# Kernel tuning notes

Hardware: AMD Instinct MI355X
Metric: run time of the kernel (lower is better)

Reference implementation:

```python
import jax, jax.numpy as jnp
import numpy as np

MARGIN = 0.8
L_INTRA = 0.1
L_INTER = 0.1
NUM_CLASSES = 64
BIG = 1e30  # finite stand-in for +/-inf so masked reductions stay NaN-free


def _pairwise(x, y):
    xn = jnp.sum(x * x, axis=1, keepdims=True)
    yn = jnp.sum(y * y, axis=1, keepdims=True)
    d2 = xn - 2.0 * (x @ y.T) + yn.T
    return jnp.sqrt(jnp.maximum(d2, 1e-8))


def _loss(anchor, positive, negative, anchor_labels, negative_labels):
    B = anchor.shape[0]
    # plain triplet term on squared distances (as in the original forward)
    pos_d2 = jnp.sum((anchor - positive) ** 2, axis=1)
    neg_d2 = jnp.sum((anchor - negative) ** 2, axis=1)
    triplet = jnp.maximum(pos_d2 - neg_d2 + MARGIN, 0.0)

    emb = jnp.concatenate([anchor, positive, negative], axis=0)                 # [3B, D]
    labels = jnp.concatenate([anchor_labels, anchor_labels, negative_labels])  # [3B]
    N = emb.shape[0]
    dist = _pairwise(emb, emb)                                                  # [3B, 3B]
    dB = dist[:B]                                                               # [B, 3B] rows for the B anchors

    idx = jnp.arange(N)
    pos_mask = (labels[None, :] == anchor_labels[:, None]) & (idx[None, :] != jnp.arange(B)[:, None])
    neg_mask = labels[None, :] != anchor_labels[:, None]
    has_pos = jnp.any(pos_mask, axis=1)
    has_neg = jnp.any(neg_mask, axis=1)

    # batch-hard mining: hardest positive (max) / hardest negative (min) per anchor
    hp = jnp.max(jnp.where(pos_mask, dB, -BIG), axis=1)
    hn = jnp.min(jnp.where(neg_mask, dB, BIG), axis=1)
    hard_valid = has_pos & has_neg
    hard_loss = jnp.where(hard_valid, jnp.maximum(hp - hn + MARGIN, 0.0), 0.0)
    hard_cnt = jnp.sum(hard_valid.astype(jnp.float32))
    hard_mean = jnp.where(hard_cnt > 0, jnp.sum(hard_loss) / jnp.maximum(hard_cnt, 1.0), 0.0)

    # semi-hard mining: for each positive distance p, min negative in (p, p + margin).
    # That min equals the smallest negative strictly greater than p (via searchsorted
    # on the sorted negatives), accepted only if it is also < p + margin.
    neg_sorted = jnp.sort(jnp.where(neg_mask, dB, BIG), axis=1)                 # [B, 3B]
    ins = jax.vmap(lambda s, q: jnp.searchsorted(s, q, side='right'))(neg_sorted, dB)
    cand = jnp.take_along_axis(neg_sorted, jnp.minimum(ins, N - 1), axis=1)
    sh_valid = pos_mask & (ins < N) & (cand < BIG) & (cand < dB + MARGIN)
    sh_loss = jnp.where(sh_valid, jnp.maximum(dB - cand + MARGIN, 0.0), 0.0)
    sh_cnt = jnp.sum(sh_valid.astype(jnp.float32))
    sh_mean = jnp.where(sh_cnt > 0, jnp.sum(sh_loss) / jnp.maximum(sh_cnt, 1.0), 0.0)

    # class-pair distance sums via one-hot projection: T[c1, c2] = sum of dist between
    # members of class c1 and c2 (diagonal = within-class sums, incl. self-pairs, as in torch)
    onehot = (labels[:, None] == jnp.arange(NUM_CLASSES)[None, :]).astype(dist.dtype)  # [3B, C]
    T = onehot.T @ dist @ onehot                                                # [C, C]
    counts = jnp.sum(onehot, axis=0)                                            # [C]
    in_anchor = jnp.zeros(NUM_CLASSES, dtype=bool).at[anchor_labels].set(True)

    intra_valid = in_anchor & (counts > 1)
    intra = jnp.sum(jnp.where(intra_valid, jnp.diag(T) / jnp.maximum(counts * (counts - 1.0), 1.0), 0.0))

    pair_n = counts[:, None] * counts[None, :]
    mean_inter = T / jnp.maximum(pair_n, 1.0)
    c = jnp.arange(NUM_CLASSES)
    pair_mask = in_anchor[:, None] & in_anchor[None, :] & (c[:, None] < c[None, :]) & (pair_n > 0)
    inter = jnp.sum(jnp.where(pair_mask, jnp.maximum(MARGIN - mean_inter, 0.0), 0.0))

    return jnp.mean(triplet) + hard_mean + sh_mean + L_INTRA * intra + L_INTER * inter


def setup_inputs() -> dict:
    key = jax.random.key(0)
    k1, k2, k3, k4, k5 = jax.random.split(key, 5)
    B, D = 1024, 2048
    anchor = jax.random.normal(k1, (B, D), dtype=jnp.float32)
    positive = jax.random.normal(k2, (B, D), dtype=jnp.float32)
    negative = jax.random.normal(k3, (B, D), dtype=jnp.float32)
    anchor_labels = jax.random.randint(k4, (B,), 0, NUM_CLASSES)
    negative_labels = jax.random.randint(k5, (B,), 0, NUM_CLASSES)
    return {"anchor": anchor, "positive": positive, "negative": negative,
            "anchor_labels": anchor_labels, "negative_labels": negative_labels}


def reference(anchor, positive, negative, anchor_labels, negative_labels):
    return _loss(anchor, positive, negative, anchor_labels, negative_labels)
```

## Files before the change

kernel.cpp:

```cpp
#include <hip/hip_runtime.h>
#include <hip/hip_bf16.h>
#include <stdint.h>

#define D_DIM 2048
#define B_DIM 1024
#define N_TOT 3072
#define NCLS 64
#define NB128 (N_TOT / 128)
#define MARGIN_F 0.8f
#define BIG_F 1e30f

typedef float f32x4 __attribute__((ext_vector_type(4)));
typedef int   i32x4 __attribute__((ext_vector_type(4)));
typedef __bf16 bf16x8 __attribute__((ext_vector_type(8)));

__device__ __forceinline__ void gld_lds16(const __bf16* g, __bf16* l) {
    __builtin_amdgcn_global_load_lds(
        (const __attribute__((address_space(1))) void*)g,
        (__attribute__((address_space(3))) void*)l,
        16, 0, 0);
}

__device__ inline float block_reduce_sum(float v, float* sred) {
    int tid = threadIdx.x;
    sred[tid] = v; __syncthreads();
    for (int s = 128; s > 0; s >>= 1) {
        if (tid < s) sred[tid] = sred[tid] + sred[tid + s];
        __syncthreads();
    }
    float r = sred[0]; __syncthreads();
    return r;
}
__device__ inline float block_sum4(float v, float* tmp4, int lane, int wave) {
    #pragma unroll
    for (int off = 32; off > 0; off >>= 1) v += __shfl_down(v, off);
    __syncthreads();
    if (lane == 0) tmp4[wave] = v;
    __syncthreads();
    return tmp4[0] + tmp4[1] + tmp4[2] + tmp4[3];
}
__device__ inline float wave_max(float v) {
    #pragma unroll
    for (int off = 32; off > 0; off >>= 1) v = fmaxf(v, __shfl_xor(v, off));
    return v;
}
__device__ inline float wave_min(float v) {
    #pragma unroll
    for (int off = 32; off > 0; off >>= 1) v = fminf(v, __shfl_xor(v, off));
    return v;
}

__device__ inline int label_of(int j, const int* __restrict__ albl, const int* __restrict__ nlbl) {
    return (j < 2 * B_DIM) ? albl[j & (B_DIM - 1)] : nlbl[j - 2 * B_DIM];
}

__device__ inline float sq8(f32x4 a, f32x4 b) {
    return a[0]*a[0] + a[1]*a[1] + a[2]*a[2] + a[3]*a[3]
         + b[0]*b[0] + b[1]*b[1] + b[2]*b[2] + b[3]*b[3];
}
__device__ inline void st_bf8(__bf16* dst, f32x4 v0, f32x4 v1) {
    bf16x8 o;
    o[0] = (__bf16)v0[0]; o[1] = (__bf16)v0[1]; o[2] = (__bf16)v0[2]; o[3] = (__bf16)v0[3];
    o[4] = (__bf16)v1[0]; o[5] = (__bf16)v1[1]; o[6] = (__bf16)v1[2]; o[7] = (__bf16)v1[3];
    *(bf16x8*)dst = o;
}

__global__ __launch_bounds__(256) void zero_kernel(
        float* __restrict__ T,
        const int* __restrict__ albl, const int* __restrict__ nlbl, int* __restrict__ lab) {
    int t = blockIdx.x * 256 + threadIdx.x;
    if (t < NCLS * NCLS) T[t] = 0.f;
    if (t < N_TOT) lab[t] = label_of(t, albl, nlbl);
}

__global__ __launch_bounds__(256) void prep_kernel(
        const float* __restrict__ A, const float* __restrict__ P, const float* __restrict__ Ng,
        __bf16* __restrict__ Eb, float* __restrict__ norms, float* __restrict__ pbT) {
    __shared__ float tmp4[4];
    int i = blockIdx.x, tid = threadIdx.x;
    int lane = tid & 63, wave = tid >> 6;
    const f32x4* a4 = (const f32x4*)(A + (size_t)i * D_DIM);
    const f32x4* p4 = (const f32x4*)(P + (size_t)i * D_DIM);
    const f32x4* n4 = (const f32x4*)(Ng + (size_t)i * D_DIM);
    f32x4 av0 = a4[tid * 2], av1 = a4[tid * 2 + 1];
    f32x4 pv0 = p4[tid * 2], pv1 = p4[tid * 2 + 1];
    f32x4 nv0 = n4[tid * 2], nv1 = n4[tid * 2 + 1];
    float sa = sq8(av0, av1), sp = sq8(pv0, pv1), sn = sq8(nv0, nv1);
    f32x4 dp0 = av0 - pv0, dp1 = av1 - pv1;
    f32x4 dn0 = av0 - nv0, dn1 = av1 - nv1;
    float pd = sq8(dp0, dp1), nd = sq8(dn0, dn1);
    st_bf8(Eb + (size_t)i * D_DIM + tid * 8, av0, av1);
    st_bf8(Eb + (size_t)(B_DIM + i) * D_DIM + tid * 8, pv0, pv1);
    st_bf8(Eb + (size_t)(2 * B_DIM + i) * D_DIM + tid * 8, nv0, nv1);
    float saT = block_sum4(sa, tmp4, lane, wave);
    float spT = block_sum4(sp, tmp4, lane, wave);
    float snT = block_sum4(sn, tmp4, lane, wave);
    float pdT = block_sum4(pd, tmp4, lane, wave);
    float ndT = block_sum4(nd, tmp4, lane, wave);
    if (tid == 0) {
        norms[i] = saT;
        norms[B_DIM + i] = spT;
        norms[2 * B_DIM + i] = snT;
        pbT[i] = fmaxf(pdT - ndT + MARGIN_F, 0.f);
    }
}

__global__ __launch_bounds__(512) void gram_gemm(
        const __bf16* __restrict__ Eb, float* __restrict__ G,
        const float* __restrict__ norms, const int* __restrict__ lab, float* __restrict__ T) {
    __shared__ __bf16 As[128 * 32] __attribute__((aligned(16)));
    __shared__ __bf16 Bs[128 * 32] __attribute__((aligned(16)));
    __shared__ float tb[NCLS * 65];
    __shared__ float rnorm[128], cnorm[128];
    __shared__ int rlabs[128], clabs[128];
    int tid = threadIdx.x, lane = tid & 63, wave = tid >> 6;
    int by = 0, rem = blockIdx.x;
    while (rem >= NB128 - by) { rem -= (NB128 - by); ++by; }
    int bx = by + rem;
    size_t row0 = (size_t)by * 128, col0 = (size_t)bx * 128;
    int wr = wave >> 2, wc = wave & 3;
    f32x4 acc[4][2];
    #pragma unroll
    for (int m = 0; m < 4; ++m)
        #pragma unroll
        for (int n = 0; n < 2; ++n) acc[m][n] = (f32x4){0.f, 0.f, 0.f, 0.f};

    if (tid < 128) { rnorm[tid] = norms[row0 + tid]; rlabs[tid] = lab[row0 + tid]; }
    else if (tid < 256) { int t = tid - 128; cnorm[t] = norms[col0 + t]; clabs[t] = lab[col0 + t]; }
    for (int x = tid; x < NCLS * 65; x += 512) tb[x] = 0.f;

    int rl = lane & 15;
    int kg = (lane >> 4) * 8;
    int srow = wave * 16 + (lane >> 2), scol = (lane & 3) * 8;
    const __bf16* gA = Eb + (row0 + srow) * D_DIM + scol;
    const __bf16* gB = Eb + (col0 + srow) * D_DIM + scol;
    __bf16* lA = &As[(wave * 16) * 32];
    __bf16* lB = &Bs[(wave * 16) * 32];

    for (int k0 = 0; k0 < D_DIM; k0 += 32) {
        __syncthreads();
        gld_lds16(gA + k0, lA);
        gld_lds16(gB + k0, lB);
        __syncthreads();
        bf16x8 af[4], bf[2];
        #pragma unroll
        for (int m = 0; m < 4; ++m)
            af[m] = *(const bf16x8*)&As[(wr * 64 + m * 16 + rl) * 32 + kg];
        #pragma unroll
        for (int n = 0; n < 2; ++n)
            bf[n] = *(const bf16x8*)&Bs[(wc * 32 + n * 16 + rl) * 32 + kg];
        #pragma unroll
        for (int m = 0; m < 4; ++m)
            #pragma unroll
            for (int n = 0; n < 2; ++n)
                acc[m][n] = __builtin_amdgcn_mfma_f32_16x16x32_bf16(af[m], bf[n], acc[m][n], 0, 0, 0);
    }
    int rg = (lane >> 4) * 4;
    bool offdiag = (by != bx);
    bool writeG = (by < 8);
    #pragma unroll
    for (int m = 0; m < 4; ++m)
        #pragma unroll
        for (int n = 0; n < 2; ++n) {
            int lcol = wc * 32 + n * 16 + rl;
            float cn = cnorm[lcol];
            int b = clabs[lcol];
            #pragma unroll
            for (int r = 0; r < 4; ++r) {
                int lrow = wr * 64 + m * 16 + rg + r;
                float g = acc[m][n][r];
                float d = sqrtf(fmaxf(rnorm[lrow] + cn - 2.f * g, 1e-8f));
                int a = rlabs[lrow];
                if (offdiag) {
                    if (a == b) atomicAdd(&tb[a * 65 + a], 2.f * d);
                    else { int lo = min(a, b), hi = max(a, b); atomicAdd(&tb[lo * 65 + hi], d); }
                } else {
                    if (a < b) atomicAdd(&tb[a * 65 + b], d);
                    else if (a == b) atomicAdd(&tb[a * 65 + a], d);
                }
                if (writeG) G[(row0 + lrow) * N_TOT + col0 + lcol] = g;
            }
        }
    __syncthreads();
    for (int x = tid; x < NCLS * NCLS; x += 512) {
        int c1 = x >> 6, c2 = x & 63;
        if (c1 <= c2) {
            float v = tb[c1 * 65 + c2];
            if (v != 0.f) atomicAdd(&T[x], v);
        }
    }
}

__global__ __launch_bounds__(256) void mirror_kernel(float* __restrict__ G) {
    __shared__ float s[64 * 65];
    int b = blockIdx.x;
    int p = b >> 2, q = b & 3;
    int bj = 0, rem = p;
    while (rem >= 7 - bj) { rem -= (7 - bj); ++bj; }
    int bi = bj + 1 + rem;
    int ti = bi * 2 + (q >> 1), tj = bj * 2 + (q & 1);
    int tid = threadIdx.x;
    int c = tid & 63, r4 = tid >> 6;
    const float* src = G + ((size_t)tj * 64) * N_TOT + (size_t)ti * 64;
    float* dst = G + ((size_t)ti * 64) * N_TOT + (size_t)tj * 64;
    #pragma unroll
    for (int rr = 0; rr < 16; ++rr) {
        int row = rr * 4 + r4;
        s[row * 65 + c] = src[(size_t)row * N_TOT + c];
    }
    __syncthreads();
    #pragma unroll
    for (int rr = 0; rr < 16; ++rr) {
        int row = rr * 4 + r4;
        dst[(size_t)row * N_TOT + c] = s[c * 65 + row];
    }
}

__global__ __launch_bounds__(512) void minev_kernel(
        const float* __restrict__ G, const float* __restrict__ norms,
        const int* __restrict__ lab, float* __restrict__ pb4) {
    __shared__ float qlist[128];
    __shared__ unsigned binmin[130];
    __shared__ float sufmin[130];
    __shared__ float hpw[8], hnw[8];
    __shared__ int pcount;
    int i = blockIdx.x, tid = threadIdx.x;
    int lane = tid & 63, wave = tid >> 6;
    if (tid == 0) pcount = 0;
    if (tid < 130) binmin[tid] = 0x7F800000u;
    __syncthreads();
    int la = lab[i];
    float ni = norms[i];
    const float* Grow = G + (size_t)i * N_TOT;
    float hp = -BIG_F, hn = BIG_F;

    f32x4 dnA, dnB;
    {
        int j = tid * 4;
        f32x4 g = *(const f32x4*)&Grow[j];
        f32x4 nj = *(const f32x4*)&norms[j];
        i32x4 lj = *(const i32x4*)&lab[j];
        f32x4 d2 = ni + nj - 2.f * g;
        float d0 = sqrtf(fmaxf(d2[0], 1e-8f));
        float d1 = sqrtf(fmaxf(d2[1], 1e-8f));
        float dd2 = sqrtf(fmaxf(d2[2], 1e-8f));
        float d3 = sqrtf(fmaxf(d2[3], 1e-8f));
        bool n0 = lj[0] != la, n1 = lj[1] != la, n2 = lj[2] != la, n3 = lj[3] != la;
        dnA = (f32x4){ n0 ? d0 : BIG_F, n1 ? d1 : BIG_F, n2 ? dd2 : BIG_F, n3 ? d3 : BIG_F };
        hn = fminf(hn, fminf(fminf(dnA[0], dnA[1]), fminf(dnA[2], dnA[3])));
        if (!n0 && j + 0 != i) { hp = fmaxf(hp, d0); int p = atomicAdd(&pcount, 1); if (p < 128) qlist[p] = d0; }
        if (!n1 && j + 1 != i) { hp = fmaxf(hp, d1); int p = atomicAdd(&pcount, 1); if (p < 128) qlist[p] = d1; }
        if (!n2 && j + 2 != i) { hp = fmaxf(hp, dd2); int p = atomicAdd(&pcount, 1); if (p < 128) qlist[p] = dd2; }
        if (!n3 && j + 3 != i) { hp = fmaxf(hp, d3); int p = atomicAdd(&pcount, 1); if (p < 128) qlist[p] = d3; }
    }
    if (tid < 256) {
        int j = 2048 + tid * 4;
        f32x4 g = *(const f32x4*)&Grow[j];
        f32x4 nj = *(const f32x4*)&norms[j];
        i32x4 lj = *(const i32x4*)&lab[j];
        f32x4 d2 = ni + nj - 2.f * g;
        float d0 = sqrtf(fmaxf(d2[0], 1e-8f));
        float d1 = sqrtf(fmaxf(d2[1], 1e-8f));
        float dd2 = sqrtf(fmaxf(d2[2], 1e-8f));
        float d3 = sqrtf(fmaxf(d2[3], 1e-8f));
        bool n0 = lj[0] != la, n1 = lj[1] != la, n2 = lj[2] != la, n3 = lj[3] != la;
        dnB = (f32x4){ n0 ? d0 : BIG_F, n1 ? d1 : BIG_F, n2 ? dd2 : BIG_F, n3 ? d3 : BIG_F };
        hn = fminf(hn, fminf(fminf(dnB[0], dnB[1]), fminf(dnB[2], dnB[3])));
        if (!n0 && j + 0 != i) { hp = fmaxf(hp, d0); int p = atomicAdd(&pcount, 1); if (p < 128) qlist[p] = d0; }
        if (!n1 && j + 1 != i) { hp = fmaxf(hp, d1); int p = atomicAdd(&pcount, 1); if (p < 128) qlist[p] = d1; }
        if (!n2 && j + 2 != i) { hp = fmaxf(hp, dd2); int p = atomicAdd(&pcount, 1); if (p < 128) qlist[p] = dd2; }
        if (!n3 && j + 3 != i) { hp = fmaxf(hp, d3); int p = atomicAdd(&pcount, 1); if (p < 128) qlist[p] = d3; }
    } else {
        dnB = (f32x4){BIG_F, BIG_F, BIG_F, BIG_F};
    }
    float hpw_ = wave_max(hp), hnw_ = wave_min(hn);
    if (lane == 0) { hpw[wave] = hpw_; hnw[wave] = hnw_; }
    __syncthreads();

    int P = min(pcount, 128);
    if (P > 0) {
        int cA0 = 0, cA1 = 0, cA2 = 0, cA3 = 0, cB0 = 0, cB1 = 0, cB2 = 0, cB3 = 0;
        for (int k = 0; k < P; ++k) {
            float qk = qlist[k];
            cA0 += (qk < dnA[0]); cA1 += (qk < dnA[1]);
            cA2 += (qk < dnA[2]); cA3 += (qk < dnA[3]);
            cB0 += (qk < dnB[0]); cB1 += (qk < dnB[1]);
            cB2 += (qk < dnB[2]); cB3 += (qk < dnB[3]);
        }
        if (dnA[0] < 1e29f) atomicMin(&binmin[cA0], __float_as_uint(dnA[0]));
        if (dnA[1] < 1e29f) atomicMin(&binmin[cA1], __float_as_uint(dnA[1]));
        if (dnA[2] < 1e29f) atomicMin(&binmin[cA2], __float_as_uint(dnA[2]));
        if (dnA[3] < 1e29f) atomicMin(&binmin[cA3], __float_as_uint(dnA[3]));
        if (dnB[0] < 1e29f) atomicMin(&binmin[cB0], __float_as_uint(dnB[0]));
        if (dnB[1] < 1e29f) atomicMin(&binmin[cB1], __float_as_uint(dnB[1]));
        if (dnB[2] < 1e29f) atomicMin(&binmin[cB2], __float_as_uint(dnB[2]));
        if (dnB[3] < 1e29f) atomicMin(&binmin[cB3], __float_as_uint(dnB[3]));
    }
    __syncthreads();

    if (wave == 0) {
        float s = 0.f, n = 0.f;
        if (P > 0) {
            int nb = P + 1;
            int nch = (nb + 63) >> 6;
            float carry = BIG_F;
            for (int ch = nch - 1; ch >= 0; --ch) {
                int idx = ch * 64 + lane;
                float v = (idx < nb) ? __uint_as_float(binmin[idx]) : BIG_F;
                #pragma unroll
                for (int off = 1; off < 64; off <<= 1)
                    v = fminf(v, __shfl_down(v, off));
                v = fminf(v, carry);
                if (idx < nb) sufmin[idx] = v;
                carry = __shfl(v, 0);
            }
            for (int base = 0; base < P; base += 64) {
                int k = base + lane;
                if (k < P) {
                    float q = qlist[k];
                    int m = 0;
                    for (int j = 0; j < P; ++j) m += (qlist[j] <= q);
                    float cand = sufmin[m];
                    if (cand < 1e29f && cand < q + MARGIN_F) { s += q - cand + MARGIN_F; n += 1.f; }
                }
            }
            #pragma unroll
            for (int off = 32; off > 0; off >>= 1) {
                s += __shfl_down(s, off);
                n += __shfl_down(n, off);
            }
        }
        if (lane == 0) {
            float hpAll = hpw[0], hnAll = hnw[0];
            #pragma unroll
            for (int w = 1; w < 8; ++w) { hpAll = fmaxf(hpAll, hpw[w]); hnAll = fminf(hnAll, hnw[w]); }
            bool valid = (P > 0 && hnAll < 1e29f);
            pb4[i * 4 + 0] = valid ? fmaxf(hpAll - hnAll + MARGIN_F, 0.f) : 0.f;
            pb4[i * 4 + 1] = valid ? 1.f : 0.f;
            pb4[i * 4 + 2] = s;
            pb4[i * 4 + 3] = n;
        }
    }
}

__global__ __launch_bounds__(256) void finalize_kernel(
        const float* __restrict__ T, const int* __restrict__ albl, const int* __restrict__ nlbl,
        const float* __restrict__ pbT, const float* __restrict__ pb4, float* __restrict__ out) {
    __shared__ int counts[NCLS];
    __shared__ int inA[NCLS];
    __shared__ float sred[256];
    int tid = threadIdx.x;
    if (tid < NCLS) { counts[tid] = 0; inA[tid] = 0; }
    __syncthreads();
    float tsum = 0.f, hsum = 0.f, hcnt = 0.f, ssum = 0.f, scnt = 0.f;
    for (int i = tid; i < B_DIM; i += 256) {
        atomicAdd(&counts[albl[i]], 2);
        inA[albl[i]] = 1;
        atomicAdd(&counts[nlbl[i]], 1);
        tsum += pbT[i];
        f32x4 p = *(const f32x4*)&pb4[i * 4];
        hsum += p[0]; hcnt += p[1]; ssum += p[2]; scnt += p[3];
    }
    __syncthreads();
    float intra = 0.f;
    if (tid < NCLS) {
        int c = tid;
        float cnt = (float)counts[c];
        if (inA[c] && counts[c] > 1)
            intra = T[c * NCLS + c] / fmaxf(cnt * (cnt - 1.f), 1.f);
    }
    float inter = 0.f;
    for (int x = tid; x < NCLS * NCLS; x += 256) {
        int c1 = x >> 6, c2 = x & 63;
        if (c1 < c2 && inA[c1] && inA[c2]) {
            float pn = (float)counts[c1] * (float)counts[c2];
            if (pn > 0.f) inter += fmaxf(MARGIN_F - T[x] / fmaxf(pn, 1.f), 0.f);
        }
    }
    float tsumA = block_reduce_sum(tsum, sred);
    float hsumA = block_reduce_sum(hsum, sred);
    float hcntA = block_reduce_sum(hcnt, sred);
    float ssumA = block_reduce_sum(ssum, sred);
    float scntA = block_reduce_sum(scnt, sred);
    float intraAll = block_reduce_sum(intra, sred);
    float interAll = block_reduce_sum(inter, sred);
    if (tid == 0) {
        float trip = tsumA / (float)B_DIM;
        float hard = (hcntA > 0.f) ? hsumA / fmaxf(hcntA, 1.f) : 0.f;
        float sh   = (scntA > 0.f) ? ssumA / fmaxf(scntA, 1.f) : 0.f;
        out[0] = trip + hard + sh + 0.1f * intraAll + 0.1f * interAll;
    }
}

extern "C" void kernel_launch(void* const* d_in, const int* in_sizes, int n_in,
                              void* d_out, int out_size, void* d_ws, size_t ws_size,
                              hipStream_t stream) {
    const float* A  = (const float*)d_in[0];
    const float* P  = (const float*)d_in[1];
    const float* Ng = (const float*)d_in[2];
    const int* albl = (const int*)d_in[3];
    const int* nlbl = (const int*)d_in[4];
    char* ws = (char*)d_ws;
    __bf16* Eb   = (__bf16*)(ws);
    float* G     = (float*)(ws + 12582912);
    float* norms = (float*)(ws + 25165824);
    float* T     = (float*)(ws + 25178112);
    int*   lab   = (int*)(ws + 25194496);
    float* pbT   = (float*)(ws + 25206784);
    float* pb4   = (float*)(ws + 25210880);
    float* out   = (float*)d_out;

    hipLaunchKernelGGL(zero_kernel, dim3(16), dim3(256), 0, stream, T, albl, nlbl, lab);
    hipLaunchKernelGGL(prep_kernel, dim3(B_DIM), dim3(256), 0, stream, A, P, Ng, Eb, norms, pbT);
    hipLaunchKernelGGL(gram_gemm, dim3(NB128 * (NB128 + 1) / 2), dim3(512), 0, stream, Eb, G, norms, lab, T);
    hipLaunchKernelGGL(mirror_kernel, dim3(28 * 4), dim3(256), 0, stream, G);
    hipLaunchKernelGGL(minev_kernel, dim3(B_DIM), dim3(512), 0, stream, G, norms, lab, pb4);
    hipLaunchKernelGGL(finalize_kernel, dim3(1), dim3(256), 0, stream, T, albl, nlbl, pbT, pb4, out);
}
```

Baseline: 203.3 us.

## Double-buffer Gram GEMM tiles with K=64 and XOR-swizzled LDS layout

Rewrites the Gram-matrix GEMM main loop to use a K-tile of 64 with two LDS buffers, so the async global-to-LDS loads for the next tile are issued while MFMAs run on the current one. The LDS layout is XOR-swizzled by row to reduce bank conflicts on fragment reads. The per-class reduction table now reuses the same 64 KB shared buffer after the loop. Barriers drop from two per 32-wide K step to one per 64-wide step, at the cost of much more LDS per block, which may lower occupancy.

Measured after the change: 193.1 us. -5.0%, faster.

```diff
diff --git a/kernel.cpp b/kernel.cpp
--- a/kernel.cpp
+++ b/kernel.cpp
@@ -108,9 +108,7 @@
 __global__ __launch_bounds__(512) void gram_gemm(
         const __bf16* __restrict__ Eb, float* __restrict__ G,
         const float* __restrict__ norms, const int* __restrict__ lab, float* __restrict__ T) {
-    __shared__ __bf16 As[128 * 32] __attribute__((aligned(16)));
-    __shared__ __bf16 Bs[128 * 32] __attribute__((aligned(16)));
-    __shared__ float tb[NCLS * 65];
+    __shared__ __align__(16) char smem[65536];
     __shared__ float rnorm[128], cnorm[128];
     __shared__ int rlabs[128], clabs[128];
     int tid = threadIdx.x, lane = tid & 63, wave = tid >> 6;
@@ -127,34 +125,69 @@
 
     if (tid < 128) { rnorm[tid] = norms[row0 + tid]; rlabs[tid] = lab[row0 + tid]; }
     else if (tid < 256) { int t = tid - 128; cnorm[t] = norms[col0 + t]; clabs[t] = lab[col0 + t]; }
+
+    int lr8 = lane >> 3, lc = lane & 7;
+    int gcol = (lc ^ lr8) * 8;
+    const __bf16* ga0 = Eb + (row0 + wave * 16 + lr8) * D_DIM + gcol;
+    const __bf16* ga1 = ga0 + 8 * D_DIM;
+    const __bf16* gb0 = Eb + (col0 + wave * 16 + lr8) * D_DIM + gcol;
+    const __bf16* gb1 = gb0 + 8 * D_DIM;
+    __bf16* sm = (__bf16*)smem;
+
+    const int nT = D_DIM / 64;
+    {
+        __bf16* Ab = sm;
+        __bf16* Bb = sm + 8192;
+        gld_lds16(ga0, Ab + (wave * 16) * 64);
+        gld_lds16(ga1, Ab + (wave * 16 + 8) * 64);
+        gld_lds16(gb0, Bb + (wave * 16) * 64);
+        gld_lds16(gb1, Bb + (wave * 16 + 8) * 64);
+    }
+    __syncthreads();
+
+    int rl = lane & 15;
+    int l7 = lane & 7;
+    int cb0 = (lane >> 4);
+    int cur = 0;
+    for (int t = 0; t < nT; ++t) {
+        if (t + 1 < nT) {
+            int k0 = (t + 1) * 64;
+            __bf16* Ab = sm + (cur ^ 1) * 16384;
+            __bf16* Bb = Ab + 8192;
+            gld_lds16(ga0 + k0, Ab + (wave * 16) * 64);
+            gld_lds16(ga1 + k0, Ab + (wave * 16 + 8) * 64);
+            gld_lds16(gb0 + k0, Bb + (wave * 16) * 64);
+            gld_lds16(gb1 + k0, Bb + (wave * 16 + 8) * 64);
+        }
+        __bf16* Ab = sm + cur * 16384;
+        __bf16* Bb = Ab + 8192;
+        #pragma unroll
+        for (int kk = 0; kk < 2; ++kk) {
+            int cb = cb0 + kk * 4;
+            bf16x8 af[4], bf[2];
+            #pragma unroll
+            for (int m = 0; m < 4; ++m) {
+                int r = wr * 64 + m * 16 + rl;
+                af[m] = *(const bf16x8*)&Ab[r * 64 + (cb ^ l7) * 8];
+            }
+            #pragma unroll
+            for (int n = 0; n < 2; ++n) {
+                int r = wc * 32 + n * 16 + rl;
+                bf[n] = *(const bf16x8*)&Bb[r * 64 + (cb ^ l7) * 8];
+            }
+            #pragma unroll
+            for (int m = 0; m < 4; ++m)
+                #pragma unroll
+                for (int n = 0; n < 2; ++n)
+                    acc[m][n] = __builtin_amdgcn_mfma_f32_16x16x32_bf16(af[m], bf[n], acc[m][n], 0, 0, 0);
+        }
+        __syncthreads();
+        cur ^= 1;
+    }
+
+    float* tb = (float*)smem;
     for (int x = tid; x < NCLS * 65; x += 512) tb[x] = 0.f;
-
-    int rl = lane & 15;
-    int kg = (lane >> 4) * 8;
-    int srow = wave * 16 + (lane >> 2), scol = (lane & 3) * 8;
-    const __bf16* gA = Eb + (row0 + srow) * D_DIM + scol;
-    const __bf16* gB = Eb + (col0 + srow) * D_DIM + scol;
-    __bf16* lA = &As[(wave * 16) * 32];
-    __bf16* lB = &Bs[(wave * 16) * 32];
-
-    for (int k0 = 0; k0 < D_DIM; k0 += 32) {
-        __syncthreads();
-        gld_lds16(gA + k0, lA);
-        gld_lds16(gB + k0, lB);
-        __syncthreads();
-        bf16x8 af[4], bf[2];
-        #pragma unroll
-        for (int m = 0; m < 4; ++m)
-            af[m] = *(const bf16x8*)&As[(wr * 64 + m * 16 + rl) * 32 + kg];
-        #pragma unroll
-        for (int n = 0; n < 2; ++n)
-            bf[n] = *(const bf16x8*)&Bs[(wc * 32 + n * 16 + rl) * 32 + kg];
-        #pragma unroll
-        for (int m = 0; m < 4; ++m)
-            #pragma unroll
-            for (int n = 0; n < 2; ++n)
-                acc[m][n] = __builtin_amdgcn_mfma_f32_16x16x32_bf16(af[m], bf[n], acc[m][n], 0, 0, 0);
-    }
+    __syncthreads();
     int rg = (lane >> 4) * 4;
     bool offdiag = (by != bx);
     bool writeG = (by < 8);
```
